# Kernel optimization log

Hardware: AMD Instinct MI355X
Metric: run time of the kernel (lower is better)

Reference implementation:

```python
import jax, jax.numpy as jnp
import numpy as np

B, T, D, R, WP, WF, NS = 32, 256, 512, 4, 8, 8, 2
N = B * T


def _build_graph():
    # Windowed dialog graph: edge j -> i for j in [i-WP, i+WF], j != i.
    # rel = (0 if same speaker else 2) + (1 if j > i else 0)
    rng = np.random.RandomState(0)
    spk = rng.randint(0, NS, size=(B, T))
    src, dst, rel = [], [], []
    for b in range(B):
        off = b * T
        for i in range(T):
            for j in range(max(0, i - WP), min(T - 1, i + WF) + 1):
                if j == i:
                    continue
                r = (0 if spk[b, j] == spk[b, i] else 2) + int(j > i)
                src.append(off + j)
                dst.append(off + i)
                rel.append(r)
    return np.array([src, dst], dtype=np.int32), np.array(rel, dtype=np.int32)


def setup_inputs() -> dict:
    key = jax.random.key(0)
    ks = jax.random.split(key, 16)
    ei, et = _build_graph()
    s = 0.02
    f32 = jnp.float32
    return {
        "x": jax.random.normal(ks[0], (B, T, D), f32),
        "edge_index": jnp.asarray(ei),
        "edge_type": jnp.asarray(et),
        # RGCNConv params (aggr='mean', root_weight=True, bias=True)
        "W_rel": jax.random.normal(ks[1], (R, D, D), f32) * s,
        "W_root": jax.random.normal(ks[2], (D, D), f32) * s,
        "b_rgcn": jnp.zeros((D,), f32),
        # TransformerConv params (heads=1, concat=True, root_weight=True)
        "Wq": jax.random.normal(ks[3], (D, D), f32) * s,
        "bq": jnp.zeros((D,), f32),
        "Wk": jax.random.normal(ks[4], (D, D), f32) * s,
        "bk": jnp.zeros((D,), f32),
        "Wv": jax.random.normal(ks[5], (D, D), f32) * s,
        "bv": jnp.zeros((D,), f32),
        "Wskip": jax.random.normal(ks[6], (D, D), f32) * s,
        "bskip": jnp.zeros((D,), f32),
        # LayerNorm params
        "gamma": jnp.ones((D,), f32),
        "beta": jnp.zeros((D,), f32),
    }


def _gnn(x, edge_index, edge_type, W_rel, W_root, b_rgcn,
         Wq, bq, Wk, bk, Wv, bv, Wskip, bskip, gamma, beta):
    nodes = x.reshape(N, D)  # all dia_len == T, so valid nodes = all nodes
    src, dst = edge_index[0], edge_index[1]

    # --- RGCNConv: per-relation linear + mean aggregation over each relation ---
    xW = jnp.einsum("nd,rde->nre", nodes, W_rel)          # [N, R, D]
    msg = xW[src, edge_type]                                # [E, D]
    comb = dst * R + edge_type                              # group (dst, rel)
    cnt = jax.ops.segment_sum(jnp.ones(src.shape, nodes.dtype), comb,
                              num_segments=N * R).reshape(N, R)
    inv = 1.0 / jnp.maximum(cnt, 1.0)
    msg = msg * inv[dst, edge_type][:, None]
    ho = jax.ops.segment_sum(msg, dst, num_segments=N) + nodes @ W_root + b_rgcn

    # --- TransformerConv (heads=1): edge attention + scatter-softmax ---
    q = ho @ Wq + bq
    k = ho @ Wk + bk
    v = ho @ Wv + bv
    logits = jnp.sum(q[dst] * k[src], axis=-1) / jnp.sqrt(jnp.asarray(D, ho.dtype))
    mx = jax.ops.segment_max(logits, dst, num_segments=N)
    mx = jnp.where(jnp.isfinite(mx), mx, 0.0)               # nodes w/o in-edges
    ex = jnp.exp(logits - mx[dst])
    den = jax.ops.segment_sum(ex, dst, num_segments=N)
    alpha = ex / jnp.maximum(den[dst], 1e-16)
    agg = jax.ops.segment_sum(alpha[:, None] * v[src], dst, num_segments=N)
    h = agg + ho @ Wskip + bskip

    h = jax.nn.leaky_relu(h, 0.01)                          # dropout = identity (eval)
    out = x + h.reshape(B, T, D)
    mu = out.mean(-1, keepdims=True)
    var = out.var(-1, keepdims=True)
    return (out - mu) / jnp.sqrt(var + 1e-5) * gamma + beta


def reference(x, edge_index, edge_type, W_rel, W_root, b_rgcn,
              Wq, bq, Wk, bk, Wv, bv, Wskip, bskip, gamma, beta):
    out = _gnn(x, edge_index, edge_type, W_rel, W_root, b_rgcn,
               Wq, bq, Wk, bk, Wv, bv, Wskip, bskip, gamma, beta)
    return out, jnp.asarray(0.0, x.dtype)  # graph_cl_loss == 0 in eval path
```

## Files before the change

### kernel.cpp

```cpp
#include <hip/hip_runtime.h>

typedef unsigned short u16;
typedef __attribute__((ext_vector_type(8))) short s16x8;
typedef __attribute__((ext_vector_type(4))) float f32x4;

__device__ __forceinline__ float bf2f(u16 u) {
  union { unsigned int i; float f; } v; v.i = ((unsigned int)u) << 16; return v.f;
}
__device__ __forceinline__ u16 f2bf(float f) {
  union { float f; unsigned int i; } v; v.f = f;
  unsigned int r = (v.i + 0x7FFFu + ((v.i >> 16) & 1u)) >> 16;
  return (u16)r;
}
__device__ __forceinline__ void async16(const void* g, void* l) {
  __builtin_amdgcn_global_load_lds((const __attribute__((address_space(1))) void*)g,
                                   (__attribute__((address_space(3))) void*)l, 16, 0, 0);
}

__global__ __launch_bounds__(256) void prep_kernel(
    const float* __restrict__ W_rel, const float* __restrict__ W_root,
    const float* __restrict__ Wq, const float* __restrict__ Wk,
    const float* __restrict__ Wv, const float* __restrict__ Wskip,
    const float* __restrict__ bq, const float* __restrict__ bk,
    const float* __restrict__ bv, const float* __restrict__ bskip,
    const float* __restrict__ x,
    u16* __restrict__ Bt1, u16* __restrict__ Bt2, float* __restrict__ bias2,
    u16* __restrict__ Acat, int Nn,
    const int* __restrict__ dst, int E, int* __restrict__ rs, int* __restrict__ re)
{
  const int b = (int)blockIdx.x;
  const int tid = threadIdx.x;
  if (b < 576) {
    __shared__ float tile[64][65];
    const float* S;
    u16* D;
    int ldD;
    long dbase;
    if (b < 320) {
      const int kt = b >> 3, et = b & 7;
      const int r0 = kt * 64, c0 = et * 64;
      S = (r0 < 2048) ? (W_rel + (long)r0 * 512 + c0)
                      : (W_root + (long)(r0 - 2048) * 512 + c0);
      D = Bt1; ldD = 2560; dbase = (long)c0 * 2560 + r0;
    } else {
      const int b2 = b - 320;
      const int jt = b2 >> 3, kt = b2 & 7;
      const int j0 = jt * 64, k0 = kt * 64;
      const int which = j0 >> 9, col0 = j0 & 511;
      const float* W = (which == 0) ? Wq : (which == 1) ? Wk : (which == 2) ? Wv : Wskip;
      S = W + (long)k0 * 512 + col0;
      D = Bt2; ldD = 512; dbase = (long)j0 * 512 + k0;
    }
    const int lc = tid & 63;
#pragma unroll
    for (int i = 0; i < 16; ++i) {
      const int r = (tid >> 6) * 16 + i;
      tile[r][lc] = S[(long)r * 512 + lc];
    }
    __syncthreads();
    const int oc2 = (tid & 31) * 2;
#pragma unroll
    for (int i = 0; i < 8; ++i) {
      const int orow = (tid >> 5) + i * 8;
      const unsigned int pk = (unsigned int)f2bf(tile[oc2][orow]) |
                              ((unsigned int)f2bf(tile[oc2 + 1][orow]) << 16);
      *(unsigned int*)(D + dbase + (long)orow * ldD + oc2) = pk;
    }
  } else if (b == 576) {
#pragma unroll
    for (int i = 0; i < 8; ++i) {
      const int j = tid + i * 256;
      const int which = j >> 9, col = j & 511;
      const float* bb = (which == 0) ? bq : (which == 1) ? bk : (which == 2) ? bv : bskip;
      bias2[j] = bb[col];
    }
  } else if (b < 8769) {
    const long u = ((long)(b - 577) * 256 + tid) * 2;
    if (u < (long)Nn * 512) {
      const float2 v = *(const float2*)(x + u);
      const unsigned int pk = (unsigned int)f2bf(v.x) | ((unsigned int)f2bf(v.y) << 16);
      *(unsigned int*)(Acat + ((long)(u >> 9)) * 2560 + 2048 + (u & 511)) = pk;
    }
  } else {
    const int e = (b - 8769) * 256 + tid;
    if (e < E) {
      const int d = dst[e];
      if (e == 0 || dst[e - 1] != d) rs[d] = e;
      if (e == E - 1 || dst[e + 1] != d) re[d] = e + 1;
    }
  }
}

__global__ __launch_bounds__(256) void aggregate_kernel(
    const float* __restrict__ x, const int* __restrict__ src,
    const int* __restrict__ etype, const int* __restrict__ rs,
    const int* __restrict__ re, u16* __restrict__ Acat)
{
  __shared__ int s_src[16];
  __shared__ int s_rel[16];
  const int q = (int)gridDim.x >> 3;
  const int bid = (int)blockIdx.x;
  const int i = (bid & 7) * q + (bid >> 3);
  const int tid = threadIdx.x;
  const int s = rs[i];
  int nE = re[i] - s;
  if (nE > 16) nE = 16;
  if (tid < nE) { s_src[tid] = src[s + tid]; s_rel[tid] = etype[s + tid]; }
  __syncthreads();

  float2 acc[4] = {};
  int cnt[4] = {0, 0, 0, 0};
  for (int t = 0; t < nE; ++t) {
    const int sj = s_src[t];
    const int rel = s_rel[t];
    const float2 v = *(const float2*)(x + (long)sj * 512 + tid * 2);
#pragma unroll
    for (int r = 0; r < 4; ++r)
      if (rel == r) { acc[r].x += v.x; acc[r].y += v.y; cnt[r]++; }
  }

  const long base = (long)i * 2560 + tid * 2;
#pragma unroll
  for (int r = 0; r < 4; ++r) {
    const float inv = 1.0f / fmaxf((float)cnt[r], 1.0f);
    const unsigned int pk = ((unsigned int)f2bf(acc[r].y * inv) << 16) | f2bf(acc[r].x * inv);
    *(unsigned int*)(Acat + base + r * 512) = pk;
  }
}

__global__ __launch_bounds__(512) void gemm_bt_kernel(
    const u16* __restrict__ A, const u16* __restrict__ Bt,
    const float* __restrict__ bias, u16* __restrict__ C,
    const int M, const int N, const int K)
{
  __shared__ u16 lds[3][2][128 * 64];
  const int tid = threadIdx.x;
  const int lane = tid & 63, wid = tid >> 6;
  const int nbn = N >> 7;
  const int q = (int)gridDim.x >> 3;
  const int bid = (int)blockIdx.x;
  const int swz = (bid & 7) * q + (bid >> 3);
  const int bm = swz / nbn, bn = swz % nbn;
  const int wr = wid >> 2, wc = wid & 3;

  f32x4 acc[4][2] = {};

  const int srow = tid >> 3;
  const int sch = tid & 7;
  const long a_row0 = (long)bm * 128;
  const long b_row0 = (long)bn * 128;
  const int lds_wbase = wid * 512;

  auto STAGE = [&](int buf, int kt) {
#pragma unroll
    for (int it = 0; it < 2; ++it) {
      const int row = it * 64 + srow;
      const int lch = sch ^ (row & 7);
      async16(A  + (a_row0 + row) * K + kt + lch * 8, &lds[buf][0][it * 4096 + lds_wbase]);
      async16(Bt + (b_row0 + row) * K + kt + lch * 8, &lds[buf][1][it * 4096 + lds_wbase]);
    }
  };

  const int nt = K >> 6;
  STAGE(0, 0);
  STAGE(1, 64);
  int bufc = 0;
  for (int t = 0; t < nt; ++t) {
    if (t + 1 < nt) { asm volatile("s_waitcnt vmcnt(4)" ::: "memory"); }
    else            { asm volatile("s_waitcnt vmcnt(0)" ::: "memory"); }
    __builtin_amdgcn_s_barrier();
    if (t + 2 < nt) {
      const int sb = (bufc == 0) ? 2 : bufc - 1;
      STAGE(sb, (t + 2) << 6);
    }
#pragma unroll
    for (int kk = 0; kk < 2; ++kk) {
      s16x8 af[4], bfr[2];
#pragma unroll
      for (int mi = 0; mi < 4; ++mi) {
        const int row = wr * 64 + mi * 16 + (lane & 15);
        const int cb = (kk * 64 + ((lane >> 4) << 4)) ^ ((row & 7) << 4);
        af[mi] = *(const s16x8*)((const char*)&lds[bufc][0][0] + row * 128 + cb);
      }
#pragma unroll
      for (int ni = 0; ni < 2; ++ni) {
        const int row = wc * 32 + ni * 16 + (lane & 15);
        const int cb = (kk * 64 + ((lane >> 4) << 4)) ^ ((row & 7) << 4);
        bfr[ni] = *(const s16x8*)((const char*)&lds[bufc][1][0] + row * 128 + cb);
      }
      __builtin_amdgcn_s_setprio(1);
#pragma unroll
      for (int mi = 0; mi < 4; ++mi)
#pragma unroll
        for (int ni = 0; ni < 2; ++ni)
          acc[mi][ni] = __builtin_amdgcn_mfma_f32_16x16x32_bf16(af[mi], bfr[ni], acc[mi][ni], 0, 0, 0);
      __builtin_amdgcn_s_setprio(0);
    }
    bufc = (bufc == 2) ? 0 : bufc + 1;
  }

#pragma unroll
  for (int mi = 0; mi < 4; ++mi) {
    const int row0 = bm * 128 + wr * 64 + mi * 16 + ((lane >> 4) << 2);
#pragma unroll
    for (int ni = 0; ni < 2; ++ni) {
      const int col = bn * 128 + wc * 32 + ni * 16 + (lane & 15);
      const float bv = bias[col];
#pragma unroll
      for (int j = 0; j < 4; ++j)
        C[(long)(row0 + j) * N + col] = f2bf(acc[mi][ni][j] + bv);
    }
  }
}

__global__ __launch_bounds__(512, 2) void gemm256_kernel(
    const u16* __restrict__ A, const u16* __restrict__ Bt,
    const float* __restrict__ bias, u16* __restrict__ C,
    const int M, const int N, const int K)
{
  __shared__ u16 lds[2][2][256 * 64];
  const int tid = threadIdx.x;
  const int lane = tid & 63, wid = tid >> 6;
  const int nbn = N >> 8;
  const int q = (int)gridDim.x >> 3;
  const int bid = (int)blockIdx.x;
  const int swz = (bid & 7) * q + (bid >> 3);
  const int bm = swz / nbn, bn = swz % nbn;
  const int wr = wid >> 2, wc = wid & 3;

  f32x4 acc[8][4] = {};

  const int srow = tid >> 3;
  const int sch = tid & 7;
  const long a_row0 = (long)bm * 256;
  const long b_row0 = (long)bn * 256;
  const int lds_wbase = wid * 512;

  auto STAGE = [&](int buf, int kt) {
#pragma unroll
    for (int it = 0; it < 4; ++it) {
      const int row = it * 64 + srow;
      const int lch = sch ^ (srow & 7);
      async16(A  + (a_row0 + row) * K + kt + lch * 8, &lds[buf][0][it * 4096 + lds_wbase]);
      async16(Bt + (b_row0 + row) * K + kt + lch * 8, &lds[buf][1][it * 4096 + lds_wbase]);
    }
  };

  const int nt = K >> 6;
  STAGE(0, 0);
  int cur = 0;
  for (int t = 0; t < nt; ++t) {
    asm volatile("s_waitcnt vmcnt(0)" ::: "memory");
    __builtin_amdgcn_s_barrier();
    s16x8 bfr[4][2];
#pragma unroll
    for (int p = 0; p < 4; ++p) {
      s16x8 af[2][2];
#pragma unroll
      for (int i2 = 0; i2 < 2; ++i2) {
        const int row = wr * 128 + (p * 2 + i2) * 16 + (lane & 15);
#pragma unroll
        for (int kk = 0; kk < 2; ++kk) {
          const int cb = (kk * 64 + ((lane >> 4) << 4)) ^ ((row & 7) << 4);
          af[i2][kk] = *(const s16x8*)((const char*)&lds[cur][0][0] + row * 128 + cb);
        }
      }
      if (p == 0) {
#pragma unroll
        for (int ni = 0; ni < 4; ++ni) {
          const int row = wc * 64 + ni * 16 + (lane & 15);
#pragma unroll
          for (int kk = 0; kk < 2; ++kk) {
            const int cb = (kk * 64 + ((lane >> 4) << 4)) ^ ((row & 7) << 4);
            bfr[ni][kk] = *(const s16x8*)((const char*)&lds[cur][1][0] + row * 128 + cb);
          }
        }
        if (t + 1 < nt) STAGE(cur ^ 1, (t + 1) << 6);
      }
      __builtin_amdgcn_s_barrier();
      asm volatile("s_waitcnt lgkmcnt(0)" ::: "memory");
      __builtin_amdgcn_sched_barrier(0);
      __builtin_amdgcn_s_setprio(1);
#pragma unroll
      for (int i2 = 0; i2 < 2; ++i2)
#pragma unroll
        for (int ni = 0; ni < 4; ++ni)
#pragma unroll
          for (int kk = 0; kk < 2; ++kk)
            acc[p * 2 + i2][ni] = __builtin_amdgcn_mfma_f32_16x16x32_bf16(
                af[i2][kk], bfr[ni][kk], acc[p * 2 + i2][ni], 0, 0, 0);
      __builtin_amdgcn_s_setprio(0);
      __builtin_amdgcn_s_barrier();
    }
    cur ^= 1;
  }

#pragma unroll
  for (int mi = 0; mi < 8; ++mi) {
    const int row0 = bm * 256 + wr * 128 + mi * 16 + ((lane >> 4) << 2);
#pragma unroll
    for (int ni = 0; ni < 4; ++ni) {
      const int col = bn * 256 + wc * 64 + ni * 16 + (lane & 15);
      const float bv = bias[col];
#pragma unroll
      for (int j = 0; j < 4; ++j)
        C[(long)(row0 + j) * N + col] = f2bf(acc[mi][ni][j] + bv);
    }
  }
}

__global__ __launch_bounds__(256) void attn_tile_kernel(
    const u16* __restrict__ qkvs, const int* __restrict__ src,
    const int* __restrict__ rs, const int* __restrict__ re,
    const float* __restrict__ x, const float* __restrict__ gamma,
    const float* __restrict__ beta, float* __restrict__ out,
    float* __restrict__ scl)
{
  __shared__ u16 Kl[48 * 512];
  __shared__ u16 Vl[48 * 512];
  __shared__ float sm[32][16];
  __shared__ int s_src[32][16];
  __shared__ int s_s0[32];
  __shared__ int s_ne[32];
  const int bid = (int)blockIdx.x;
  const int tid = threadIdx.x;
  const int lane = tid & 63, wid = tid >> 6;
  const int tile = (bid & 7) * ((int)gridDim.x >> 3) + (bid >> 3);
  const int i0 = tile * 32;
  if (bid == 0 && tid == 0) scl[0] = 0.0f;

  const int blo = i0 & ~255;
  const int lo = max(i0 - 8, blo);
  const int hi = min(i0 + 40, blo + 256);
  const int R = hi - lo;

  if (tid < 32) {
    const int s0 = rs[i0 + tid];
    int ne = re[i0 + tid] - s0;
    if (ne > 16) ne = 16;
    s_s0[tid] = s0;
    s_ne[tid] = ne;
  }
  __syncthreads();
  for (int idx = tid; idx < 512; idx += 256) {
    const int d = idx >> 4, e = idx & 15;
    if (e < s_ne[d]) s_src[d][e] = src[s_s0[d] + e] - lo;
  }
#pragma unroll
  for (int k = 0; k < 12; ++k) {
    const int r = wid * 12 + k;
    if (r < R) {
      const long gb = (long)(lo + r) * 2048;
      async16(qkvs + gb + 512  + ((lane ^ (r & 3)) * 8), &Kl[r * 512 + lane * 8]);
      async16(qkvs + gb + 1024 + lane * 8,               &Vl[r * 512 + lane * 8]);
    }
  }
  asm volatile("s_waitcnt vmcnt(0)" ::: "memory");
  __syncthreads();

  const int g16 = lane & 15;
  const int eg  = lane >> 4;

#pragma unroll 1
  for (int j = 0; j < 8; ++j) {
    const int d = wid * 8 + j;
    const int i = i0 + d;
    const int ne = s_ne[d];
    float qv[32];
#pragma unroll
    for (int c = 0; c < 4; ++c) {
      const s16x8 q8 = *(const s16x8*)(qkvs + (long)i * 2048 + c * 128 + g16 * 8);
#pragma unroll
      for (int u = 0; u < 8; ++u) qv[c * 8 + u] = bf2f((u16)q8[u]);
    }
#pragma unroll
    for (int round = 0; round < 4; ++round) {
      const int e = round * 4 + eg;
      float dp = 0.f;
      if (e < ne) {
        const int r = s_src[d][e];
        const int rx = r & 3;
#pragma unroll
        for (int c = 0; c < 4; ++c) {
          const s16x8 k8 = *(const s16x8*)&Kl[r * 512 + (((c * 16 + g16) ^ rx) * 8)];
#pragma unroll
          for (int u = 0; u < 8; ++u) dp += qv[c * 8 + u] * bf2f((u16)k8[u]);
        }
      }
#pragma unroll
      for (int m = 1; m <= 8; m <<= 1) dp += __shfl_xor(dp, m);
      if (g16 == 0 && e < ne) sm[d][e] = dp * 0.04419417382415922f;
    }
    {
      const float v = (lane < 16 && lane < ne) ? sm[d][lane] : -1e30f;
      float mx = v;
#pragma unroll
      for (int m = 1; m <= 8; m <<= 1) mx = fmaxf(mx, __shfl_xor(mx, m));
      const float ex = (lane < 16 && lane < ne) ? expf(v - mx) : 0.f;
      float den = ex;
#pragma unroll
      for (int m = 1; m <= 8; m <<= 1) den += __shfl_xor(den, m);
      if (lane < 16 && lane < ne) sm[d][lane] = ex / fmaxf(den, 1e-16f);
    }
  }

  const int d8 = lane * 8;
#pragma unroll 1
  for (int j = 0; j < 8; ++j) {
    const int d = wid * 8 + j;
    const int i = i0 + d;
    const int ne = s_ne[d];
    float a[8] = {};
    for (int e = 0; e < ne; ++e) {
      const float al = sm[d][e];
      const int r = s_src[d][e];
      const s16x8 v8 = *(const s16x8*)&Vl[r * 512 + d8];
#pragma unroll
      for (int u = 0; u < 8; ++u) a[u] += al * bf2f((u16)v8[u]);
    }
    const s16x8 sk8 = *(const s16x8*)(qkvs + (long)i * 2048 + 1536 + d8);
    const float4 x0 = *(const float4*)(x + (long)i * 512 + d8);
    const float4 x1 = *(const float4*)(x + (long)i * 512 + d8 + 4);
    float o[8];
    float s = 0.f, s2 = 0.f;
#pragma unroll
    for (int u = 0; u < 8; ++u) {
      float h = a[u] + bf2f((u16)sk8[u]);
      h = (h > 0.f) ? h : 0.01f * h;
      const float xx = (u < 4) ? ((const float*)&x0)[u] : ((const float*)&x1)[u - 4];
      o[u] = xx + h;
      s += o[u];
      s2 += o[u] * o[u];
    }
#pragma unroll
    for (int m = 32; m >= 1; m >>= 1) { s += __shfl_xor(s, m); s2 += __shfl_xor(s2, m); }
    const float mean = s * (1.f / 512.f);
    const float var = s2 * (1.f / 512.f) - mean * mean;
    const float rstd = rsqrtf(var + 1e-5f);
    const float4 g0 = *(const float4*)(gamma + d8), g1 = *(const float4*)(gamma + d8 + 4);
    const float4 b0 = *(const float4*)(beta + d8),  b1 = *(const float4*)(beta + d8 + 4);
    float4 r0, r1;
    r0.x = (o[0] - mean) * rstd * g0.x + b0.x;
    r0.y = (o[1] - mean) * rstd * g0.y + b0.y;
    r0.z = (o[2] - mean) * rstd * g0.z + b0.z;
    r0.w = (o[3] - mean) * rstd * g0.w + b0.w;
    r1.x = (o[4] - mean) * rstd * g1.x + b1.x;
    r1.y = (o[5] - mean) * rstd * g1.y + b1.y;
    r1.z = (o[6] - mean) * rstd * g1.z + b1.z;
    r1.w = (o[7] - mean) * rstd * g1.w + b1.w;
    *(float4*)(out + (long)i * 512 + d8) = r0;
    *(float4*)(out + (long)i * 512 + d8 + 4) = r1;
  }
}

extern "C" void kernel_launch(void* const* d_in, const int* in_sizes, int n_in,
                              void* d_out, int out_size, void* d_ws, size_t ws_size,
                              hipStream_t stream) {
  const float* x      = (const float*)d_in[0];
  const int*   ei     = (const int*)d_in[1];
  const int*   et     = (const int*)d_in[2];
  const float* W_rel  = (const float*)d_in[3];
  const float* W_root = (const float*)d_in[4];
  const float* b_rgcn = (const float*)d_in[5];
  const float* Wq     = (const float*)d_in[6];
  const float* bq     = (const float*)d_in[7];
  const float* Wk     = (const float*)d_in[8];
  const float* bk     = (const float*)d_in[9];
  const float* Wv     = (const float*)d_in[10];
  const float* bv     = (const float*)d_in[11];
  const float* Wskip  = (const float*)d_in[12];
  const float* bskip  = (const float*)d_in[13];
  const float* gamma  = (const float*)d_in[14];
  const float* beta   = (const float*)d_in[15];
  const int E  = in_sizes[2];
  const int Nn = in_sizes[0] / 512;
  const int* srcA = ei;
  const int* dstA = ei + E;

  char* p = (char*)d_ws;
  u16* Acat   = (u16*)p;   p += (size_t)Nn * 2560 * 2;
  u16* Bt1    = (u16*)p;   p += (size_t)512 * 2560 * 2;
  u16* Bt2    = (u16*)p;   p += (size_t)2048 * 512 * 2;
  float* bias2= (float*)p; p += (size_t)2048 * 4;
  u16* ho     = (u16*)p;   p += (size_t)Nn * 512 * 2;
  u16* qkvs   = (u16*)p;   p += (size_t)Nn * 2048 * 2;
  int* rs     = (int*)p;   p += (size_t)Nn * 4;
  int* re     = (int*)p;   p += (size_t)Nn * 4;

  {
    const int FB = (E + 255) / 256;
    const int blocks = 8769 + FB;
    prep_kernel<<<blocks, 256, 0, stream>>>(W_rel, W_root, Wq, Wk, Wv, Wskip,
                                            bq, bk, bv, bskip, x, Bt1, Bt2, bias2, Acat, Nn,
                                            dstA, E, rs, re);
  }
  aggregate_kernel<<<Nn, 256, 0, stream>>>(x, srcA, et, rs, re, Acat);
  gemm_bt_kernel<<<(Nn / 128) * (512 >> 7), 512, 0, stream>>>(Acat, Bt1, b_rgcn, ho, Nn, 512, 2560);
  gemm256_kernel<<<(Nn / 256) * (2048 >> 8), 512, 0, stream>>>(ho, Bt2, bias2, qkvs, Nn, 2048, 512);
  attn_tile_kernel<<<Nn / 32, 256, 0, stream>>>(qkvs, srcA, rs, re, x, gamma, beta,
                                                (float*)d_out, (float*)d_out + (size_t)Nn * 512);
}
```

Before: 129.2 us.

## Gather neighbors from bf16 copy, vectorize conversion, double-buffer RGCN GEMM

The aggregation kernel now gathers neighbor rows from the bf16 copy of x already stored in Acat, halving gather bytes compared with reading fp32 x. The prep kernel converts four floats per thread instead of two, halving the conversion blocks. The RGCN GEMM drops from triple to double buffering with a full vmcnt(0) wait each step, and adds a launch bound of 4 blocks to raise occupancy. The trade-off is less load/compute overlap in the GEMM, plus bf16-rounded inputs to the mean aggregation, which slightly changes numerics.

Result: no change. 131.0 us (+1.4%).

```diff
diff --git a/kernel.cpp b/kernel.cpp
--- a/kernel.cpp
+++ b/kernel.cpp
@@ -74,15 +74,17 @@
       const float* bb = (which == 0) ? bq : (which == 1) ? bk : (which == 2) ? bv : bskip;
       bias2[j] = bb[col];
     }
-  } else if (b < 8769) {
-    const long u = ((long)(b - 577) * 256 + tid) * 2;
+  } else if (b < 4673) {
+    const long u = ((long)(b - 577) * 256 + tid) * 4;
     if (u < (long)Nn * 512) {
-      const float2 v = *(const float2*)(x + u);
-      const unsigned int pk = (unsigned int)f2bf(v.x) | ((unsigned int)f2bf(v.y) << 16);
-      *(unsigned int*)(Acat + ((long)(u >> 9)) * 2560 + 2048 + (u & 511)) = pk;
+      const float4 v = *(const float4*)(x + u);
+      const unsigned int p0 = (unsigned int)f2bf(v.x) | ((unsigned int)f2bf(v.y) << 16);
+      const unsigned int p1 = (unsigned int)f2bf(v.z) | ((unsigned int)f2bf(v.w) << 16);
+      unsigned int* dp = (unsigned int*)(Acat + ((long)(u >> 9)) * 2560 + 2048 + (u & 511));
+      dp[0] = p0; dp[1] = p1;
     }
   } else {
-    const int e = (b - 8769) * 256 + tid;
+    const int e = (b - 4673) * 256 + tid;
     if (e < E) {
       const int d = dst[e];
       if (e == 0 || dst[e - 1] != d) rs[d] = e;
@@ -92,7 +94,7 @@
 }
 
 __global__ __launch_bounds__(256) void aggregate_kernel(
-    const float* __restrict__ x, const int* __restrict__ src,
+    const u16* __restrict__ Acat_ro, const int* __restrict__ src,
     const int* __restrict__ etype, const int* __restrict__ rs,
     const int* __restrict__ re, u16* __restrict__ Acat)
 {
@@ -113,10 +115,11 @@
   for (int t = 0; t < nE; ++t) {
     const int sj = s_src[t];
     const int rel = s_rel[t];
-    const float2 v = *(const float2*)(x + (long)sj * 512 + tid * 2);
+    const unsigned int pk = *(const unsigned int*)(Acat_ro + (long)sj * 2560 + 2048 + tid * 2);
+    const float vx = bf2f((u16)pk), vy = bf2f((u16)(pk >> 16));
 #pragma unroll
     for (int r = 0; r < 4; ++r)
-      if (rel == r) { acc[r].x += v.x; acc[r].y += v.y; cnt[r]++; }
+      if (rel == r) { acc[r].x += vx; acc[r].y += vy; cnt[r]++; }
   }
 
   const long base = (long)i * 2560 + tid * 2;
@@ -128,12 +131,12 @@
   }
 }
 
-__global__ __launch_bounds__(512) void gemm_bt_kernel(
+__global__ __launch_bounds__(512, 4) void gemm_bt_kernel(
     const u16* __restrict__ A, const u16* __restrict__ Bt,
     const float* __restrict__ bias, u16* __restrict__ C,
     const int M, const int N, const int K)
 {
-  __shared__ u16 lds[3][2][128 * 64];
+  __shared__ u16 lds[2][2][128 * 64];
   const int tid = threadIdx.x;
   const int lane = tid & 63, wid = tid >> 6;
   const int nbn = N >> 7;
@@ -163,16 +166,11 @@
 
   const int nt = K >> 6;
   STAGE(0, 0);
-  STAGE(1, 64);
-  int bufc = 0;
+  int cur = 0;
   for (int t = 0; t < nt; ++t) {
-    if (t + 1 < nt) { asm volatile("s_waitcnt vmcnt(4)" ::: "memory"); }
-    else            { asm volatile("s_waitcnt vmcnt(0)" ::: "memory"); }
+    asm volatile("s_waitcnt vmcnt(0)" ::: "memory");
     __builtin_amdgcn_s_barrier();
-    if (t + 2 < nt) {
-      const int sb = (bufc == 0) ? 2 : bufc - 1;
-      STAGE(sb, (t + 2) << 6);
-    }
+    if (t + 1 < nt) STAGE(cur ^ 1, (t + 1) << 6);
 #pragma unroll
     for (int kk = 0; kk < 2; ++kk) {
       s16x8 af[4], bfr[2];
@@ -180,13 +178,13 @@
       for (int mi = 0; mi < 4; ++mi) {
         const int row = wr * 64 + mi * 16 + (lane & 15);
         const int cb = (kk * 64 + ((lane >> 4) << 4)) ^ ((row & 7) << 4);
-        af[mi] = *(const s16x8*)((const char*)&lds[bufc][0][0] + row * 128 + cb);
+        af[mi] = *(const s16x8*)((const char*)&lds[cur][0][0] + row * 128 + cb);
       }
 #pragma unroll
       for (int ni = 0; ni < 2; ++ni) {
         const int row = wc * 32 + ni * 16 + (lane & 15);
         const int cb = (kk * 64 + ((lane >> 4) << 4)) ^ ((row & 7) << 4);
-        bfr[ni] = *(const s16x8*)((const char*)&lds[bufc][1][0] + row * 128 + cb);
+        bfr[ni] = *(const s16x8*)((const char*)&lds[cur][1][0] + row * 128 + cb);
       }
       __builtin_amdgcn_s_setprio(1);
 #pragma unroll
@@ -196,7 +194,7 @@
           acc[mi][ni] = __builtin_amdgcn_mfma_f32_16x16x32_bf16(af[mi], bfr[ni], acc[mi][ni], 0, 0, 0);
       __builtin_amdgcn_s_setprio(0);
     }
-    bufc = (bufc == 2) ? 0 : bufc + 1;
+    cur ^= 1;
   }
 
 #pragma unroll
@@ -489,12 +487,12 @@
 
   {
     const int FB = (E + 255) / 256;
-    const int blocks = 8769 + FB;
+    const int blocks = 4673 + FB;
     prep_kernel<<<blocks, 256, 0, stream>>>(W_rel, W_root, Wq, Wk, Wv, Wskip,
                                             bq, bk, bv, bskip, x, Bt1, Bt2, bias2, Acat, Nn,
                                             dstA, E, rs, re);
   }
-  aggregate_kernel<<<Nn, 256, 0, stream>>>(x, srcA, et, rs, re, Acat);
+  aggregate_kernel<<<Nn, 256, 0, stream>>>(Acat, srcA, et, rs, re, Acat);
   gemm_bt_kernel<<<(Nn / 128) * (512 >> 7), 512, 0, stream>>>(Acat, Bt1, b_rgcn, ho, Nn, 512, 2560);
   gemm256_kernel<<<(Nn / 256) * (2048 >> 8), 512, 0, stream>>>(ho, Bt2, bias2, qkvs, Nn, 2048, 512);
   attn_tile_kernel<<<Nn / 32, 256, 0, stream>>>(qkvs, srcA, rs, re, x, gamma, beta,
```
